# Kernel tuning notes

Hardware: AMD Instinct MI355X
Metric: run time of the kernel (lower is better)

Reference implementation:

```python
import jax, jax.numpy as jnp
import numpy as np

NUM_SEGMENTS = 24  # static max number of sentence segments (matches segment_ids fill_max)


def setup_inputs() -> dict:
    key = jax.random.key(0)
    k1, k2, k3 = jax.random.split(key, 3)
    B, L, S, D = 32, 4, 512, 768
    embeddings = jax.random.normal(k1, (B, L, S, D), dtype=jnp.float32)
    # word index of each subword token (sorted, as produced by left-to-right '##' merging)
    token_group_ids = jnp.sort(jax.random.randint(k2, (B, S), 0, 300), axis=1).astype(jnp.int32)
    # sentence-segment id of each (aggregated) word position (sorted, from '.'-cumsum)
    segment_ids = jnp.sort(jax.random.randint(k3, (B, S), 0, NUM_SEGMENTS), axis=1).astype(jnp.int32)
    return {"embeddings": embeddings, "token_group_ids": token_group_ids, "segment_ids": segment_ids}


def _segsum(data, seg_ids, num_segments):
    # data: [S, D], seg_ids: [S] -> [num_segments, D]
    return jax.ops.segment_sum(data, seg_ids, num_segments=num_segments)


def reference(embeddings, token_group_ids, segment_ids):
    B, L, S, D = embeddings.shape
    # --- aggregate_tokens: scatter-sum subword embeddings into word slots, padded to S ---
    # vmap over batch and layer; word capacity = S (original pads agg_embs back to num_words)
    per_layer = jax.vmap(_segsum, in_axes=(0, None, None))          # over L
    per_batch = jax.vmap(per_layer, in_axes=(0, 0, None))           # over B
    word_layer = per_batch(embeddings, token_group_ids, S)          # [B, L, S, D]
    # --- sentence embedding: mean over (padded) word axis, then sum over layers ---
    sent_embeddings = word_layer.mean(axis=2).sum(axis=1)           # [B, D]
    # --- word embedding: sum over layers (aggregate_method='sum') ---
    word_embeddings = word_layer.sum(axis=1)                        # [B, S, D]
    # --- aggregate_segments: scatter-sum word embeddings into sentence segments ---
    seg_embeddings = jax.vmap(_segsum, in_axes=(0, 0, None))(
        word_embeddings, segment_ids, NUM_SEGMENTS)                 # [B, G, D]
    seg_num = segment_ids.max(axis=1) + 1                           # [B]
    seg_mask = jnp.arange(NUM_SEGMENTS)[None, :] >= seg_num[:, None]  # True = padded segment
    return word_embeddings, sent_embeddings, seg_embeddings, seg_mask
```

## Files before the change

kernel.cpp:

```cpp
#include <hip/hip_runtime.h>

#define BB 32
#define LL 4
#define SS 512
#define DD 768
#define D4 (DD / 4)
#define GG 24

typedef float floatx4 __attribute__((ext_vector_type(4)));

#define WB_STRIDE (SS + 1)
#define SB_STRIDE (GG + 1)

__global__ __launch_bounds__(SS) void bounds_kernel(
    const int* __restrict__ tg, const int* __restrict__ sg,
    int* __restrict__ wb, int* __restrict__ sb, float* __restrict__ mask)
{
    __shared__ int ltg[SS];
    __shared__ int lsg[SS];
    const int b = blockIdx.x;
    const int t = threadIdx.x;
    ltg[t] = tg[b * SS + t];
    lsg[t] = sg[b * SS + t];
    __syncthreads();

    {
        int v = t, lo = 0, hi = SS;
        while (lo < hi) { int m = (lo + hi) >> 1; if (ltg[m] < v) lo = m + 1; else hi = m; }
        wb[b * WB_STRIDE + t] = lo;
        if (t == 0) wb[b * WB_STRIDE + SS] = SS;
    }
    if (t <= GG) {
        int v = t, lo = 0, hi = SS;
        while (lo < hi) { int m = (lo + hi) >> 1; if (lsg[m] < v) lo = m + 1; else hi = m; }
        sb[b * SB_STRIDE + t] = lo;
    }
    if (t < GG) {
        const int seg_num = lsg[SS - 1] + 1;
        mask[b * GG + t] = (t >= seg_num) ? 1.0f : 0.0f;
    }
}

__global__ __launch_bounds__(D4) void fused_agg_kernel(
    const floatx4* __restrict__ emb, const int* __restrict__ wb,
    const int* __restrict__ sb,
    floatx4* __restrict__ word, floatx4* __restrict__ seg)
{
    const int t = blockIdx.x;
    const int b = blockIdx.y;
    const int d = threadIdx.x;
    const int glo = sb[b * SB_STRIDE + t];
    const int ghi = sb[b * SB_STRIDE + t + 1];

    floatx4 seg_acc = (floatx4)(0.0f);
    for (int g = glo; g < ghi; ++g) {
        const int lo = wb[b * WB_STRIDE + g];
        const int hi = wb[b * WB_STRIDE + g + 1];
        floatx4 wacc = (floatx4)(0.0f);
        for (int s = lo; s < hi; ++s) {
#pragma unroll
            for (int l = 0; l < LL; ++l) {
                wacc += __builtin_nontemporal_load(
                    &emb[((size_t)((b * LL + l) * SS + s)) * D4 + d]);
            }
        }
        word[((size_t)(b * SS + g)) * D4 + d] = wacc;
        seg_acc += wacc;
    }
    seg[((size_t)(b * GG + t)) * D4 + d] = seg_acc;
}

__global__ __launch_bounds__(D4) void sent_kernel(
    const floatx4* __restrict__ seg, floatx4* __restrict__ sent)
{
    const int b = blockIdx.x;
    const int d = threadIdx.x;
    floatx4 acc = (floatx4)(0.0f);
#pragma unroll
    for (int t = 0; t < GG; ++t) {
        acc += seg[((size_t)(b * GG + t)) * D4 + d];
    }
    acc *= (1.0f / (float)SS);
    sent[(size_t)b * D4 + d] = acc;
}

extern "C" void kernel_launch(void* const* d_in, const int* in_sizes, int n_in,
                              void* d_out, int out_size, void* d_ws, size_t ws_size,
                              hipStream_t stream) {
    const float* emb = (const float*)d_in[0];
    const int*   tg  = (const int*)d_in[1];
    const int*   sg  = (const int*)d_in[2];

    float* out  = (float*)d_out;
    float* word = out;
    float* sent = word + (size_t)BB * SS * DD;
    float* seg  = sent + (size_t)BB * DD;
    float* mask = seg  + (size_t)BB * GG * DD;

    int* wb = (int*)d_ws;
    int* sb = wb + BB * WB_STRIDE;

    bounds_kernel<<<BB, SS, 0, stream>>>(tg, sg, wb, sb, mask);
    fused_agg_kernel<<<dim3(GG, BB), D4, 0, stream>>>(
        (const floatx4*)emb, wb, sb, (floatx4*)word, (floatx4*)seg);
    sent_kernel<<<BB, D4, 0, stream>>>((const floatx4*)seg, (floatx4*)sent);
}
```

Baseline: 302.7 us.

## Split segment aggregation across four word-strided blocks with partial sums

Result: no change. 302.8 us (+0.0%).

```diff
diff --git a/kernel.cpp b/kernel.cpp
--- a/kernel.cpp
+++ b/kernel.cpp
@@ -6,11 +6,13 @@
 #define DD 768
 #define D4 (DD / 4)
 #define GG 24
+#define PP 4
 
 typedef float floatx4 __attribute__((ext_vector_type(4)));
 
 #define WB_STRIDE (SS + 1)
 #define SB_STRIDE (GG + 1)
+
 
 __global__ __launch_bounds__(SS) void bounds_kernel(
     const int* __restrict__ tg, const int* __restrict__ sg,
@@ -44,16 +46,17 @@
 __global__ __launch_bounds__(D4) void fused_agg_kernel(
     const floatx4* __restrict__ emb, const int* __restrict__ wb,
     const int* __restrict__ sb,
-    floatx4* __restrict__ word, floatx4* __restrict__ seg)
+    floatx4* __restrict__ word, floatx4* __restrict__ partial)
 {
     const int t = blockIdx.x;
     const int b = blockIdx.y;
+    const int p = blockIdx.z;
     const int d = threadIdx.x;
     const int glo = sb[b * SB_STRIDE + t];
     const int ghi = sb[b * SB_STRIDE + t + 1];
 
     floatx4 seg_acc = (floatx4)(0.0f);
-    for (int g = glo; g < ghi; ++g) {
+    for (int g = glo + p; g < ghi; g += PP) {
         const int lo = wb[b * WB_STRIDE + g];
         const int hi = wb[b * WB_STRIDE + g + 1];
         floatx4 wacc = (floatx4)(0.0f);
@@ -67,21 +70,28 @@
         word[((size_t)(b * SS + g)) * D4 + d] = wacc;
         seg_acc += wacc;
     }
-    seg[((size_t)(b * GG + t)) * D4 + d] = seg_acc;
+    partial[((size_t)((p * BB + b) * GG + t)) * D4 + d] = seg_acc;
 }
 
-__global__ __launch_bounds__(D4) void sent_kernel(
-    const floatx4* __restrict__ seg, floatx4* __restrict__ sent)
+__global__ __launch_bounds__(D4) void finish_kernel(
+    const floatx4* __restrict__ partial,
+    floatx4* __restrict__ seg, floatx4* __restrict__ sent)
 {
     const int b = blockIdx.x;
     const int d = threadIdx.x;
-    floatx4 acc = (floatx4)(0.0f);
+    floatx4 sent_acc = (floatx4)(0.0f);
 #pragma unroll
     for (int t = 0; t < GG; ++t) {
-        acc += seg[((size_t)(b * GG + t)) * D4 + d];
+        floatx4 s = (floatx4)(0.0f);
+#pragma unroll
+        for (int p = 0; p < PP; ++p) {
+            s += partial[((size_t)((p * BB + b) * GG + t)) * D4 + d];
+        }
+        seg[((size_t)(b * GG + t)) * D4 + d] = s;
+        sent_acc += s;
     }
-    acc *= (1.0f / (float)SS);
-    sent[(size_t)b * D4 + d] = acc;
+    sent_acc *= (1.0f / (float)SS);
+    sent[(size_t)b * D4 + d] = sent_acc;
 }
 
 extern "C" void kernel_launch(void* const* d_in, const int* in_sizes, int n_in,
@@ -99,9 +109,13 @@
 
     int* wb = (int*)d_ws;
     int* sb = wb + BB * WB_STRIDE;
+    size_t int_words = (size_t)BB * WB_STRIDE + (size_t)BB * SB_STRIDE;
+    int_words = (int_words + 3) & ~(size_t)3;
+    float* partial = (float*)d_ws + int_words;
 
     bounds_kernel<<<BB, SS, 0, stream>>>(tg, sg, wb, sb, mask);
-    fused_agg_kernel<<<dim3(GG, BB), D4, 0, stream>>>(
-        (const floatx4*)emb, wb, sb, (floatx4*)word, (floatx4*)seg);
-    sent_kernel<<<BB, D4, 0, stream>>>((const floatx4*)seg, (floatx4*)sent);
+    fused_agg_kernel<<<dim3(GG, BB, PP), D4, 0, stream>>>(
+        (const floatx4*)emb, wb, sb, (floatx4*)word, (floatx4*)partial);
+    finish_kernel<<<BB, D4, 0, stream>>>(
+        (const floatx4*)partial, (floatx4*)seg, (floatx4*)sent);
 }
```
